# Performance work log

Hardware: AMD Instinct MI355X
Metric: run time of the kernel (lower is better)

Reference implementation:

```python
import jax, jax.numpy as jnp
import numpy as np

N_HEAD = 16

def setup_inputs() -> dict:
    key = jax.random.key(0)
    k1, k2, k3, k4, k5 = jax.random.split(key, 5)
    B, T, C = 8, 2048, 1024
    hs = C // N_HEAD  # 64
    return {
        "ids": jax.random.normal(k1, (B, T, C), dtype=jnp.float32),
        "qkv_w": jax.random.normal(k2, (3 * hs, C), dtype=jnp.float32) * (C ** -0.5),
        "qkv_b": jax.random.normal(k3, (3 * hs,), dtype=jnp.float32) * 0.02,
        "proj_w": jax.random.normal(k4, (C, C), dtype=jnp.float32) * (C ** -0.5),
        "proj_b": jax.random.normal(k5, (C,), dtype=jnp.float32) * 0.02,
    }

def reference(ids, qkv_w, qkv_b, proj_w, proj_b):
    B, T, C = ids.shape
    hs = qkv_w.shape[0] // 3  # head_size
    # All heads share the same qkv Linear (input is replicated per-head in the
    # original), so compute one head and tile at the end.
    qkv = ids @ qkv_w.T + qkv_b                      # [B,T,3*hs]
    q, k, v = jnp.split(qkv, 3, axis=-1)             # each [B,T,hs]
    wei = jnp.einsum('btd,bsd->bts', q, k)           # [B,T,T]
    tril = jnp.tril(jnp.ones((T, T), dtype=bool))
    wei = jnp.where(tril, wei, jnp.float32(0.0))     # causal mask (no softmax)
    out_h = jnp.einsum('bts,bsd->btd', wei, v)       # [B,T,hs]
    out = jnp.tile(out_h, (1, 1, N_HEAD))            # identical heads concatenated
    return out @ proj_w.T + proj_b                   # [B,T,C]
```

## Files before the change

### kernel.cpp

```cpp
#include <hip/hip_runtime.h>
#include <hip/hip_bf16.h>

#define Bsz 8
#define Tsz 2048
#define Csz 1024
#define HSsz 64
#define NQ 192

typedef __attribute__((ext_vector_type(8))) short short8v;
typedef __attribute__((ext_vector_type(4))) float f32x4;
typedef unsigned short ushortT;
typedef unsigned int uintT;

__device__ __forceinline__ unsigned int f2bf(float f) {
    union { float f; unsigned int u; } v; v.f = f;
    return (v.u + 0x7fffu + ((v.u >> 16) & 1u)) >> 16;
}

__device__ __forceinline__ unsigned int pk2bf(float lo, float hi) {
    union { __hip_bfloat162 h2; unsigned int u; } cv;
    cv.h2 = __float22bfloat162_rn(float2{lo, hi});
    return cv.u;
}

__global__ __launch_bounds__(256) void k_prep(const float* __restrict__ qw,
                                              const float* __restrict__ pw,
                                              ushortT* __restrict__ wB,
                                              ushortT* __restrict__ w2a) {
    const int blk = blockIdx.x;
    if (blk < 96) {
        int idx = blk * 256 + threadIdx.x;
        int l = idx & 63;
        int ksjt = idx >> 6;
        int jt = ksjt % 12, ks = ksjt / 12;
        int j = jt * 16 + (l & 15);
        int k = ks * 32 + (l >> 4) * 8;
        const float* src = &qw[j * Csz + k];
        float4 a = *(const float4*)src;
        float4 b = *(const float4*)(src + 4);
        uint4 o;
        o.x = f2bf(a.x) | (f2bf(a.y) << 16);
        o.y = f2bf(a.z) | (f2bf(a.w) << 16);
        o.z = f2bf(b.x) | (f2bf(b.y) << 16);
        o.w = f2bf(b.z) | (f2bf(b.w) << 16);
        *(uint4*)&wB[(size_t)idx * 8] = o;
    } else {
        int idx = (blk - 96) * 256 + threadIdx.x;
        int l = idx & 63;
        int rest = idx >> 6;
        int m = rest & 63, ks = rest >> 6;
        int c = m * 16 + (l & 15);
        int d0 = ks * 32 + (l >> 4) * 8;
        float s0 = 0, s1 = 0, s2 = 0, s3 = 0, s4 = 0, s5 = 0, s6 = 0, s7 = 0;
#pragma unroll
        for (int hh = 0; hh < 16; ++hh) {
            const float* p = &pw[c * Csz + hh * HSsz + d0];
            float4 x = *(const float4*)p;
            float4 y = *(const float4*)(p + 4);
            s0 += x.x; s1 += x.y; s2 += x.z; s3 += x.w;
            s4 += y.x; s5 += y.y; s6 += y.z; s7 += y.w;
        }
        uint4 o;
        o.x = f2bf(s0) | (f2bf(s1) << 16);
        o.y = f2bf(s2) | (f2bf(s3) << 16);
        o.z = f2bf(s4) | (f2bf(s5) << 16);
        o.w = f2bf(s6) | (f2bf(s7) << 16);
        *(uint4*)&w2a[(size_t)idx * 8] = o;
    }
}

__global__ __launch_bounds__(512, 4) void k_qkv_mfma(const float* __restrict__ ids,
                                                     const ushortT* __restrict__ wB,
                                                     const float* __restrict__ bias,
                                                     ushortT* __restrict__ Qf,
                                                     ushortT* __restrict__ Kf,
                                                     ushortT* __restrict__ Vf) {
    __shared__ float sA[2][32 * 68];
    uintT* Lqk = (uintT*)&sA[0][0];
    uintT* Lv  = Lqk + 32 * 68;

    const int tid = threadIdx.x;
    const int wv  = tid >> 6;
    const int l   = tid & 63;
    const int wm  = wv >> 2;
    const int wn  = wv & 3;
    const int lg  = l >> 4, ll = l & 15;

    const int row0 = blockIdx.x * 32;

    const int srow = tid >> 4;
    const int scol = (tid & 15) * 4;
    const float* gsrc = ids + (size_t)(row0 + srow) * Csz + scol;

    const int afrow = wm * 16 + ll;

    f32x4 acc[3];
    acc[0] = acc[1] = acc[2] = (f32x4){0.f, 0.f, 0.f, 0.f};

    float4 st = *(const float4*)gsrc;

    const ushortT* bbase_p = wB + ((size_t)(wn * 3) * 64 + l) * 8;

    for (int c = 0; c < 16; ++c) {
        float* bufp = &sA[c & 1][0];
        *(float4*)&bufp[srow * 68 + scol] = st;
        if (c < 15) st = *(const float4*)(gsrc + (c + 1) * 64);
        __syncthreads();

        const ushortT* bp = bbase_p + (size_t)(2 * c) * 6144;
        short8v b00 = *(const short8v*)(bp);
        short8v b01 = *(const short8v*)(bp + 512);
        short8v b02 = *(const short8v*)(bp + 1024);
        short8v b10 = *(const short8v*)(bp + 6144);
        short8v b11 = *(const short8v*)(bp + 6144 + 512);
        short8v b12 = *(const short8v*)(bp + 6144 + 1024);

        const float* ap = &bufp[afrow * 68 + lg * 8];
        float4 a00 = *(const float4*)(ap);
        float4 a01 = *(const float4*)(ap + 4);
        float4 a10 = *(const float4*)(ap + 32);
        float4 a11 = *(const float4*)(ap + 36);

        union { short8v s; unsigned int u[4]; } af0, af1;
        af0.u[0] = pk2bf(a00.x, a00.y); af0.u[1] = pk2bf(a00.z, a00.w);
        af0.u[2] = pk2bf(a01.x, a01.y); af0.u[3] = pk2bf(a01.z, a01.w);
        af1.u[0] = pk2bf(a10.x, a10.y); af1.u[1] = pk2bf(a10.z, a10.w);
        af1.u[2] = pk2bf(a11.x, a11.y); af1.u[3] = pk2bf(a11.z, a11.w);

        acc[0] = __builtin_amdgcn_mfma_f32_16x16x32_bf16(af0.s, b00, acc[0], 0, 0, 0);
        acc[1] = __builtin_amdgcn_mfma_f32_16x16x32_bf16(af0.s, b01, acc[1], 0, 0, 0);
        acc[2] = __builtin_amdgcn_mfma_f32_16x16x32_bf16(af0.s, b02, acc[2], 0, 0, 0);
        acc[0] = __builtin_amdgcn_mfma_f32_16x16x32_bf16(af1.s, b10, acc[0], 0, 0, 0);
        acc[1] = __builtin_amdgcn_mfma_f32_16x16x32_bf16(af1.s, b11, acc[1], 0, 0, 0);
        acc[2] = __builtin_amdgcn_mfma_f32_16x16x32_bf16(af1.s, b12, acc[2], 0, 0, 0);

        __syncthreads();
    }

    const int crow_l = wm * 16 + lg * 4;
    ushortT* L16 = (ushortT*)Lqk;
#pragma unroll
    for (int n = 0; n < 3; ++n) {
        const int jb = wn * 3 + n;
        const int j  = jb * 16 + ll;
        const float bj = bias[j];
        float v0 = acc[n][0] + bj, v1 = acc[n][1] + bj;
        float v2 = acc[n][2] + bj, v3 = acc[n][3] + bj;
        if (jb < 8) {
            ushortT* p = &L16[crow_l * 136 + j];
            p[0]   = (ushortT)f2bf(v0);
            p[136] = (ushortT)f2bf(v1);
            p[272] = (ushortT)f2bf(v2);
            p[408] = (ushortT)f2bf(v3);
        } else {
            uintT* p = &Lv[(j - 128) * 20 + (crow_l >> 1)];
            p[0] = pk2bf(v0, v1);
            p[1] = pk2bf(v2, v3);
        }
    }
    __syncthreads();

    const int l2 = tid & 63, ll2 = l2 & 15, lg2 = l2 >> 4;
    if (tid < 256) {
        const int ks = (tid >> 6) & 1, m = tid >> 7;
        uint4 q = *(const uint4*)&Lqk[(m * 16 + ll2) * 68 + ks * 16 + lg2 * 4];
        *(uint4*)&Qf[(((size_t)(row0 >> 4) + m) * 2 + ks) * 512 + l2 * 8] = q;
        const int n = tid >> 6;
        uint4 v = *(const uint4*)&Lv[(n * 16 + ll2) * 20 + lg2 * 4];
        const int bb = row0 >> 11, s32 = (row0 >> 5) & 63;
        *(uint4*)&Vf[((((size_t)bb * 64 + s32) * 4 + n) * 64 + l2) * 8] = v;
    } else {
        const int ks = (tid >> 6) & 1, m = (tid >> 7) & 1;
        uint4 k = *(const uint4*)&Lqk[(m * 16 + ll2) * 68 + 32 + ks * 16 + lg2 * 4];
        *(uint4*)&Kf[(((size_t)(row0 >> 4) + m) * 2 + ks) * 512 + l2 * 8] = k;
    }
}

__global__ __launch_bounds__(256, 3) void k_attn_mfma(const ushortT* __restrict__ Qf,
                                                      const ushortT* __restrict__ Kf,
                                                      const ushortT* __restrict__ Vf,
                                                      ushortT* __restrict__ hf) {
    __shared__ uintT su[4 * 2 * 16 * 36];
    __shared__ float s_o[4][32 * 68];

    const int tid = threadIdx.x;
    const int w  = tid >> 6;
    const int l  = tid & 63;
    const int lg = l >> 4;
    const int ll = l & 15;

    const int u = blockIdx.x;
    const int b = u / 48;
    const int r = u - b * 48;

    int si, sub, nsub;
    const bool heavy = (r < 32);
    if (heavy) { si = 63 - r; sub = w; nsub = 4; }
    else {
        const int rr = r - 32;
        si = (w < 2) ? (31 - rr) : rr;
        sub = w & 1; nsub = 2;
    }
    const int nT  = (si >> 1) + 1;
    const int qn  = nT / nsub, rem = nT % nsub;
    const int t0  = sub * qn + (sub < rem ? sub : rem);
    const int cnt = qn + (sub < rem ? 1 : 0);

    const int gq = b * 128 + si * 2;

    short8v qf[2][2];
#pragma unroll
    for (int mt = 0; mt < 2; ++mt)
#pragma unroll
        for (int ks = 0; ks < 2; ++ks)
            qf[mt][ks] = *(const short8v*)&Qf[(((size_t)gq + mt) * 2 + ks) * 512 + l * 8];

    f32x4 oacc[2][4];
#pragma unroll
    for (int mt = 0; mt < 2; ++mt)
#pragma unroll
        for (int n = 0; n < 4; ++n) oacc[mt][n] = (f32x4){0.f, 0.f, 0.f, 0.f};

    for (int tile = t0; tile < t0 + cnt; ++tile) {
        const int gs = b * 128 + tile * 4;
        short8v kf[4][2];
#pragma unroll
        for (int ms = 0; ms < 4; ++ms) {
            const ushortT* kp = &Kf[(((size_t)gs + ms) * 2) * 512 + l * 8];
            kf[ms][0] = *(const short8v*)kp;
            kf[ms][1] = *(const short8v*)(kp + 512);
        }
        f32x4 sacc[4][2];
#pragma unroll
        for (int ms = 0; ms < 4; ++ms)
#pragma unroll
            for (int mt = 0; mt < 2; ++mt) sacc[ms][mt] = (f32x4){0.f, 0.f, 0.f, 0.f};
#pragma unroll
        for (int ms = 0; ms < 4; ++ms)
#pragma unroll
            for (int mt = 0; mt < 2; ++mt) {
                sacc[ms][mt] = __builtin_amdgcn_mfma_f32_16x16x32_bf16(kf[ms][0], qf[mt][0], sacc[ms][mt], 0, 0, 0);
                sacc[ms][mt] = __builtin_amdgcn_mfma_f32_16x16x32_bf16(kf[ms][1], qf[mt][1], sacc[ms][mt], 0, 0, 0);
            }
        if (tile == nT - 1) {
#pragma unroll
            for (int ms = 0; ms < 4; ++ms)
#pragma unroll
                for (int mt = 0; mt < 2; ++mt) {
                    const int tg = si * 32 + mt * 16 + ll;
#pragma unroll
                    for (int rr2 = 0; rr2 < 4; ++rr2) {
                        int sg = tile * 64 + ms * 16 + 4 * lg + rr2;
                        if (sg > tg) sacc[ms][mt][rr2] = 0.f;
                    }
                }
        }
#pragma unroll
        for (int mt = 0; mt < 2; ++mt)
#pragma unroll
            for (int ms = 0; ms < 4; ++ms) {
                uint2 pk;
                pk.x = pk2bf(sacc[ms][mt][0], sacc[ms][mt][1]);
                pk.y = pk2bf(sacc[ms][mt][2], sacc[ms][mt][3]);
                *(uint2*)&su[((w * 2 + mt) * 16 + ll) * 36 + ms * 8 + 2 * lg] = pk;
            }
        union { uint4 u4; short8v s; } pa[2][2];
#pragma unroll
        for (int mt = 0; mt < 2; ++mt)
#pragma unroll
            for (int h = 0; h < 2; ++h)
                pa[mt][h].u4 = *(const uint4*)&su[((w * 2 + mt) * 16 + ll) * 36 + h * 16 + lg * 4];

        const int gv = b * 64 + tile * 2;
        short8v vf[2][4];
#pragma unroll
        for (int h = 0; h < 2; ++h)
#pragma unroll
            for (int n = 0; n < 4; ++n)
                vf[h][n] = *(const short8v*)&Vf[((((size_t)gv + h) * 4 + n) * 64 + l) * 8];
#pragma unroll
        for (int mt = 0; mt < 2; ++mt)
#pragma unroll
            for (int n = 0; n < 4; ++n) {
                oacc[mt][n] = __builtin_amdgcn_mfma_f32_16x16x32_bf16(pa[mt][0].s, vf[0][n], oacc[mt][n], 0, 0, 0);
                oacc[mt][n] = __builtin_amdgcn_mfma_f32_16x16x32_bf16(pa[mt][1].s, vf[1][n], oacc[mt][n], 0, 0, 0);
            }
    }

#pragma unroll
    for (int mt = 0; mt < 2; ++mt)
#pragma unroll
        for (int n = 0; n < 4; ++n)
#pragma unroll
            for (int rr2 = 0; rr2 < 4; ++rr2)
                s_o[w][(mt * 16 + 4 * lg + rr2) * 68 + 16 * n + ll] = oacc[mt][n][rr2];
    __syncthreads();

    const int l2 = tid & 63, ll2 = l2 & 15, lg2 = l2 >> 4;
    const int ks = (tid >> 6) & 1, mt = tid >> 7;
    const int t = mt * 16 + ll2, dd = ks * 32 + lg2 * 8;
    if (heavy) {
        float4 A = {0, 0, 0, 0}, B2 = {0, 0, 0, 0};
#pragma unroll
        for (int w2 = 0; w2 < 4; ++w2) {
            const float4 x = *(const float4*)&s_o[w2][t * 68 + dd];
            const float4 y = *(const float4*)&s_o[w2][t * 68 + dd + 4];
            A.x += x.x; A.y += x.y; A.z += x.z; A.w += x.w;
            B2.x += y.x; B2.y += y.y; B2.z += y.z; B2.w += y.w;
        }
        uint4 o;
        o.x = pk2bf(A.x, A.y);  o.y = pk2bf(A.z, A.w);
        o.z = pk2bf(B2.x, B2.y); o.w = pk2bf(B2.z, B2.w);
        *(uint4*)&hf[(((size_t)(b * 128 + si * 2) + mt) * 2 + ks) * 512 + l2 * 8] = o;
    } else {
        const int rr = r - 32;
        const int sa = 31 - rr, sb = rr;
        float4 A = {0, 0, 0, 0}, B2 = {0, 0, 0, 0};
#pragma unroll
        for (int w2 = 0; w2 < 2; ++w2) {
            const float4 x = *(const float4*)&s_o[w2][t * 68 + dd];
            const float4 y = *(const float4*)&s_o[w2][t * 68 + dd + 4];
            A.x += x.x; A.y += x.y; A.z += x.z; A.w += x.w;
            B2.x += y.x; B2.y += y.y; B2.z += y.z; B2.w += y.w;
        }
        uint4 o;
        o.x = pk2bf(A.x, A.y);  o.y = pk2bf(A.z, A.w);
        o.z = pk2bf(B2.x, B2.y); o.w = pk2bf(B2.z, B2.w);
        *(uint4*)&hf[(((size_t)(b * 128 + sa * 2) + mt) * 2 + ks) * 512 + l2 * 8] = o;
        float4 C = {0, 0, 0, 0}, D2 = {0, 0, 0, 0};
#pragma unroll
        for (int w2 = 2; w2 < 4; ++w2) {
            const float4 x = *(const float4*)&s_o[w2][t * 68 + dd];
            const float4 y = *(const float4*)&s_o[w2][t * 68 + dd + 4];
            C.x += x.x; C.y += x.y; C.z += x.z; C.w += x.w;
            D2.x += y.x; D2.y += y.y; D2.z += y.z; D2.w += y.w;
        }
        uint4 o2;
        o2.x = pk2bf(C.x, C.y);  o2.y = pk2bf(C.z, C.w);
        o2.z = pk2bf(D2.x, D2.y); o2.w = pk2bf(D2.z, D2.w);
        *(uint4*)&hf[(((size_t)(b * 128 + sb * 2) + mt) * 2 + ks) * 512 + l2 * 8] = o2;
    }
}

__global__ __launch_bounds__(256) void k_proj_mfma(const ushortT* __restrict__ hf,
                                                   const ushortT* __restrict__ w2a,
                                                   const float* __restrict__ pb,
                                                   float* __restrict__ out) {
    const int tid = threadIdx.x;
    const int w = tid >> 6, l = tid & 63;
    const int t0 = blockIdx.x * 16;
    const size_t M = blockIdx.x;

    short8v hb0 = *(const short8v*)&hf[(M * 2 + 0) * 512 + l * 8];
    short8v hb1 = *(const short8v*)&hf[(M * 2 + 1) * 512 + l * 8];

    const int row = (l >> 4) * 4;
    const int tcol = l & 15;
    const size_t outrow = (size_t)(t0 + tcol) * Csz;

#pragma unroll 2
    for (int m = w * 16; m < w * 16 + 16; ++m) {
        const ushortT* ap = w2a + (size_t)(m * 64 + l) * 8;
        short8v a0 = *(const short8v*)ap;
        short8v a1 = *(const short8v*)(ap + 32768);
        f32x4 acc = (f32x4){0.f, 0.f, 0.f, 0.f};
        acc = __builtin_amdgcn_mfma_f32_16x16x32_bf16(a0, hb0, acc, 0, 0, 0);
        acc = __builtin_amdgcn_mfma_f32_16x16x32_bf16(a1, hb1, acc, 0, 0, 0);
        const int c0 = m * 16 + row;
        const float4 pv = *(const float4*)&pb[c0];
        float4 o;
        o.x = acc[0] + pv.x; o.y = acc[1] + pv.y;
        o.z = acc[2] + pv.z; o.w = acc[3] + pv.w;
        *(float4*)&out[outrow + c0] = o;
    }
}

extern "C" void kernel_launch(void* const* d_in, const int* in_sizes, int n_in,
                              void* d_out, int out_size, void* d_ws, size_t ws_size,
                              hipStream_t stream) {
    const float* ids    = (const float*)d_in[0];
    const float* qkv_w  = (const float*)d_in[1];
    const float* qkv_b  = (const float*)d_in[2];
    const float* proj_w = (const float*)d_in[3];
    const float* proj_b = (const float*)d_in[4];
    float* out = (float*)d_out;

    ushortT* Qf  = (ushortT*)d_ws;
    ushortT* Kf  = Qf + 16384 * HSsz;
    ushortT* Vf  = Kf + 16384 * HSsz;
    ushortT* hf  = Vf + 16384 * HSsz;
    ushortT* wB  = hf + 16384 * HSsz;
    ushortT* w2a = wB + 196608;

    hipLaunchKernelGGL(k_prep,      dim3(128),  dim3(256), 0, stream, qkv_w, proj_w, wB, w2a);
    hipLaunchKernelGGL(k_qkv_mfma,  dim3(512),  dim3(512), 0, stream, ids, wB, qkv_b, Qf, Kf, Vf);
    hipLaunchKernelGGL(k_attn_mfma, dim3(384),  dim3(256), 0, stream, Qf, Kf, Vf, hf);
    hipLaunchKernelGGL(k_proj_mfma, dim3(1024), dim3(256), 0, stream, hf, w2a, proj_b, out);
}
```

Before: 62.81 us.

## Fuse output projection into attention kernel and widen QKV K-chunks

The output projection now runs inside the attention kernel. Each block reduces its per-wave partial outputs into bf16 MFMA fragments held in registers and multiplies them directly by the projection weights. This removes the intermediate hf buffer round trip through global memory and one kernel launch. Separately, the QKV GEMM now stages 128-column chunks with a single barrier per iteration, halving loop trips and barriers. The cost is that the large fp32 output store is now spread over only 384 attention blocks instead of 1024 dedicated blocks, which may reduce parallelism for the store-bound projection.

```diff
diff --git a/kernel.cpp b/kernel.cpp
--- a/kernel.cpp
+++ b/kernel.cpp
@@ -75,7 +75,7 @@
                                                      ushortT* __restrict__ Qf,
                                                      ushortT* __restrict__ Kf,
                                                      ushortT* __restrict__ Vf) {
-    __shared__ float sA[2][32 * 68];
+    __shared__ float sA[2][32 * 132];
     uintT* Lqk = (uintT*)&sA[0][0];
     uintT* Lv  = Lqk + 32 * 68;
 
@@ -89,7 +89,7 @@
     const int row0 = blockIdx.x * 32;
 
     const int srow = tid >> 4;
-    const int scol = (tid & 15) * 4;
+    const int scol = (tid & 15) * 8;
     const float* gsrc = ids + (size_t)(row0 + srow) * Csz + scol;
 
     const int afrow = wm * 16 + ll;
@@ -97,45 +97,41 @@
     f32x4 acc[3];
     acc[0] = acc[1] = acc[2] = (f32x4){0.f, 0.f, 0.f, 0.f};
 
-    float4 st = *(const float4*)gsrc;
+    float4 st0 = *(const float4*)gsrc;
+    float4 st1 = *(const float4*)(gsrc + 4);
 
     const ushortT* bbase_p = wB + ((size_t)(wn * 3) * 64 + l) * 8;
 
-    for (int c = 0; c < 16; ++c) {
+    for (int c = 0; c < 8; ++c) {
         float* bufp = &sA[c & 1][0];
-        *(float4*)&bufp[srow * 68 + scol] = st;
-        if (c < 15) st = *(const float4*)(gsrc + (c + 1) * 64);
+        float* wp = &bufp[srow * 132 + scol];
+        *(float4*)wp = st0;
+        *(float4*)(wp + 4) = st1;
         __syncthreads();
-
-        const ushortT* bp = bbase_p + (size_t)(2 * c) * 6144;
-        short8v b00 = *(const short8v*)(bp);
-        short8v b01 = *(const short8v*)(bp + 512);
-        short8v b02 = *(const short8v*)(bp + 1024);
-        short8v b10 = *(const short8v*)(bp + 6144);
-        short8v b11 = *(const short8v*)(bp + 6144 + 512);
-        short8v b12 = *(const short8v*)(bp + 6144 + 1024);
-
-        const float* ap = &bufp[afrow * 68 + lg * 8];
-        float4 a00 = *(const float4*)(ap);
-        float4 a01 = *(const float4*)(ap + 4);
-        float4 a10 = *(const float4*)(ap + 32);
-        float4 a11 = *(const float4*)(ap + 36);
-
-        union { short8v s; unsigned int u[4]; } af0, af1;
-        af0.u[0] = pk2bf(a00.x, a00.y); af0.u[1] = pk2bf(a00.z, a00.w);
-        af0.u[2] = pk2bf(a01.x, a01.y); af0.u[3] = pk2bf(a01.z, a01.w);
-        af1.u[0] = pk2bf(a10.x, a10.y); af1.u[1] = pk2bf(a10.z, a10.w);
-        af1.u[2] = pk2bf(a11.x, a11.y); af1.u[3] = pk2bf(a11.z, a11.w);
-
-        acc[0] = __builtin_amdgcn_mfma_f32_16x16x32_bf16(af0.s, b00, acc[0], 0, 0, 0);
-        acc[1] = __builtin_amdgcn_mfma_f32_16x16x32_bf16(af0.s, b01, acc[1], 0, 0, 0);
-        acc[2] = __builtin_amdgcn_mfma_f32_16x16x32_bf16(af0.s, b02, acc[2], 0, 0, 0);
-        acc[0] = __builtin_amdgcn_mfma_f32_16x16x32_bf16(af1.s, b10, acc[0], 0, 0, 0);
-        acc[1] = __builtin_amdgcn_mfma_f32_16x16x32_bf16(af1.s, b11, acc[1], 0, 0, 0);
-        acc[2] = __builtin_amdgcn_mfma_f32_16x16x32_bf16(af1.s, b12, acc[2], 0, 0, 0);
-
-        __syncthreads();
-    }
+        if (c < 7) {
+            st0 = *(const float4*)(gsrc + (c + 1) * 128);
+            st1 = *(const float4*)(gsrc + (c + 1) * 128 + 4);
+        }
+#pragma unroll
+        for (int kk = 0; kk < 4; ++kk) {
+            const ushortT* bp = bbase_p + (size_t)(4 * c + kk) * 6144;
+            short8v b0 = *(const short8v*)(bp);
+            short8v b1 = *(const short8v*)(bp + 512);
+            short8v b2 = *(const short8v*)(bp + 1024);
+
+            const float* ap = &bufp[afrow * 132 + kk * 32 + lg * 8];
+            float4 a0 = *(const float4*)ap;
+            float4 a1 = *(const float4*)(ap + 4);
+            union { short8v s; unsigned int u[4]; } af;
+            af.u[0] = pk2bf(a0.x, a0.y); af.u[1] = pk2bf(a0.z, a0.w);
+            af.u[2] = pk2bf(a1.x, a1.y); af.u[3] = pk2bf(a1.z, a1.w);
+
+            acc[0] = __builtin_amdgcn_mfma_f32_16x16x32_bf16(af.s, b0, acc[0], 0, 0, 0);
+            acc[1] = __builtin_amdgcn_mfma_f32_16x16x32_bf16(af.s, b1, acc[1], 0, 0, 0);
+            acc[2] = __builtin_amdgcn_mfma_f32_16x16x32_bf16(af.s, b2, acc[2], 0, 0, 0);
+        }
+    }
+    __syncthreads();
 
     const int crow_l = wm * 16 + lg * 4;
     ushortT* L16 = (ushortT*)Lqk;
@@ -176,10 +172,12 @@
     }
 }
 
-__global__ __launch_bounds__(256, 3) void k_attn_mfma(const ushortT* __restrict__ Qf,
+__global__ __launch_bounds__(256, 3) void k_attn_proj(const ushortT* __restrict__ Qf,
                                                       const ushortT* __restrict__ Kf,
                                                       const ushortT* __restrict__ Vf,
-                                                      ushortT* __restrict__ hf) {
+                                                      const ushortT* __restrict__ w2a,
+                                                      const float* __restrict__ pb,
+                                                      float* __restrict__ out) {
     __shared__ uintT su[4 * 2 * 16 * 36];
     __shared__ float s_o[4][32 * 68];
 
@@ -296,82 +294,52 @@
                 s_o[w][(mt * 16 + 4 * lg + rr2) * 68 + 16 * n + ll] = oacc[mt][n][rr2];
     __syncthreads();
 
-    const int l2 = tid & 63, ll2 = l2 & 15, lg2 = l2 >> 4;
-    const int ks = (tid >> 6) & 1, mt = tid >> 7;
-    const int t = mt * 16 + ll2, dd = ks * 32 + lg2 * 8;
-    if (heavy) {
-        float4 A = {0, 0, 0, 0}, B2 = {0, 0, 0, 0};
-#pragma unroll
-        for (int w2 = 0; w2 < 4; ++w2) {
-            const float4 x = *(const float4*)&s_o[w2][t * 68 + dd];
-            const float4 y = *(const float4*)&s_o[w2][t * 68 + dd + 4];
-            A.x += x.x; A.y += x.y; A.z += x.z; A.w += x.w;
-            B2.x += y.x; B2.y += y.y; B2.z += y.z; B2.w += y.w;
-        }
-        uint4 o;
-        o.x = pk2bf(A.x, A.y);  o.y = pk2bf(A.z, A.w);
-        o.z = pk2bf(B2.x, B2.y); o.w = pk2bf(B2.z, B2.w);
-        *(uint4*)&hf[(((size_t)(b * 128 + si * 2) + mt) * 2 + ks) * 512 + l2 * 8] = o;
-    } else {
+    int pstrip, nsum, wb0, mstart, mcount;
+    if (heavy) { pstrip = si; nsum = 4; wb0 = 0; mstart = w * 16; mcount = 16; }
+    else {
         const int rr = r - 32;
-        const int sa = 31 - rr, sb = rr;
-        float4 A = {0, 0, 0, 0}, B2 = {0, 0, 0, 0};
-#pragma unroll
-        for (int w2 = 0; w2 < 2; ++w2) {
-            const float4 x = *(const float4*)&s_o[w2][t * 68 + dd];
-            const float4 y = *(const float4*)&s_o[w2][t * 68 + dd + 4];
-            A.x += x.x; A.y += x.y; A.z += x.z; A.w += x.w;
-            B2.x += y.x; B2.y += y.y; B2.z += y.z; B2.w += y.w;
-        }
-        uint4 o;
-        o.x = pk2bf(A.x, A.y);  o.y = pk2bf(A.z, A.w);
-        o.z = pk2bf(B2.x, B2.y); o.w = pk2bf(B2.z, B2.w);
-        *(uint4*)&hf[(((size_t)(b * 128 + sa * 2) + mt) * 2 + ks) * 512 + l2 * 8] = o;
-        float4 C = {0, 0, 0, 0}, D2 = {0, 0, 0, 0};
-#pragma unroll
-        for (int w2 = 2; w2 < 4; ++w2) {
-            const float4 x = *(const float4*)&s_o[w2][t * 68 + dd];
-            const float4 y = *(const float4*)&s_o[w2][t * 68 + dd + 4];
-            C.x += x.x; C.y += x.y; C.z += x.z; C.w += x.w;
-            D2.x += y.x; D2.y += y.y; D2.z += y.z; D2.w += y.w;
-        }
-        uint4 o2;
-        o2.x = pk2bf(C.x, C.y);  o2.y = pk2bf(C.z, C.w);
-        o2.z = pk2bf(D2.x, D2.y); o2.w = pk2bf(D2.z, D2.w);
-        *(uint4*)&hf[(((size_t)(b * 128 + sb * 2) + mt) * 2 + ks) * 512 + l2 * 8] = o2;
-    }
-}
-
-__global__ __launch_bounds__(256) void k_proj_mfma(const ushortT* __restrict__ hf,
-                                                   const ushortT* __restrict__ w2a,
-                                                   const float* __restrict__ pb,
-                                                   float* __restrict__ out) {
-    const int tid = threadIdx.x;
-    const int w = tid >> 6, l = tid & 63;
-    const int t0 = blockIdx.x * 16;
-    const size_t M = blockIdx.x;
-
-    short8v hb0 = *(const short8v*)&hf[(M * 2 + 0) * 512 + l * 8];
-    short8v hb1 = *(const short8v*)&hf[(M * 2 + 1) * 512 + l * 8];
-
-    const int row = (l >> 4) * 4;
-    const int tcol = l & 15;
-    const size_t outrow = (size_t)(t0 + tcol) * Csz;
-
-#pragma unroll 2
-    for (int m = w * 16; m < w * 16 + 16; ++m) {
+        pstrip = (w < 2) ? (31 - rr) : rr;
+        nsum = 2; wb0 = (w < 2) ? 0 : 2;
+        mstart = (w & 1) * 32; mcount = 32;
+    }
+
+    union { short8v s; unsigned int u[4]; } hbf[2][2];
+#pragma unroll
+    for (int mt = 0; mt < 2; ++mt)
+#pragma unroll
+        for (int ks = 0; ks < 2; ++ks) {
+            float4 A = {0.f, 0.f, 0.f, 0.f}, B2 = {0.f, 0.f, 0.f, 0.f};
+            for (int w2 = wb0; w2 < wb0 + nsum; ++w2) {
+                const float* p = &s_o[w2][(mt * 16 + ll) * 68 + ks * 32 + lg * 8];
+                const float4 x = *(const float4*)p;
+                const float4 y = *(const float4*)(p + 4);
+                A.x += x.x; A.y += x.y; A.z += x.z; A.w += x.w;
+                B2.x += y.x; B2.y += y.y; B2.z += y.z; B2.w += y.w;
+            }
+            hbf[mt][ks].u[0] = pk2bf(A.x, A.y);
+            hbf[mt][ks].u[1] = pk2bf(A.z, A.w);
+            hbf[mt][ks].u[2] = pk2bf(B2.x, B2.y);
+            hbf[mt][ks].u[3] = pk2bf(B2.z, B2.w);
+        }
+
+    const int gt = b * Tsz + pstrip * 32;
+    const int crow = lg * 4;
+#pragma unroll 4
+    for (int m = mstart; m < mstart + mcount; ++m) {
         const ushortT* ap = w2a + (size_t)(m * 64 + l) * 8;
         short8v a0 = *(const short8v*)ap;
         short8v a1 = *(const short8v*)(ap + 32768);
-        f32x4 acc = (f32x4){0.f, 0.f, 0.f, 0.f};
-        acc = __builtin_amdgcn_mfma_f32_16x16x32_bf16(a0, hb0, acc, 0, 0, 0);
-        acc = __builtin_amdgcn_mfma_f32_16x16x32_bf16(a1, hb1, acc, 0, 0, 0);
-        const int c0 = m * 16 + row;
-        const float4 pv = *(const float4*)&pb[c0];
-        float4 o;
-        o.x = acc[0] + pv.x; o.y = acc[1] + pv.y;
-        o.z = acc[2] + pv.z; o.w = acc[3] + pv.w;
-        *(float4*)&out[outrow + c0] = o;
+        const float4 pv = *(const float4*)&pb[m * 16 + crow];
+#pragma unroll
+        for (int mt = 0; mt < 2; ++mt) {
+            f32x4 acc = (f32x4){0.f, 0.f, 0.f, 0.f};
+            acc = __builtin_amdgcn_mfma_f32_16x16x32_bf16(a0, hbf[mt][0].s, acc, 0, 0, 0);
+            acc = __builtin_amdgcn_mfma_f32_16x16x32_bf16(a1, hbf[mt][1].s, acc, 0, 0, 0);
+            float4 o;
+            o.x = acc[0] + pv.x; o.y = acc[1] + pv.y;
+            o.z = acc[2] + pv.z; o.w = acc[3] + pv.w;
+            *(float4*)&out[(size_t)(gt + mt * 16 + ll) * Csz + m * 16 + crow] = o;
+        }
     }
 }
 
@@ -388,12 +356,10 @@
     ushortT* Qf  = (ushortT*)d_ws;
     ushortT* Kf  = Qf + 16384 * HSsz;
     ushortT* Vf  = Kf + 16384 * HSsz;
-    ushortT* hf  = Vf + 16384 * HSsz;
-    ushortT* wB  = hf + 16384 * HSsz;
+    ushortT* wB  = Vf + 16384 * HSsz;
     ushortT* w2a = wB + 196608;
 
-    hipLaunchKernelGGL(k_prep,      dim3(128),  dim3(256), 0, stream, qkv_w, proj_w, wB, w2a);
-    hipLaunchKernelGGL(k_qkv_mfma,  dim3(512),  dim3(512), 0, stream, ids, wB, qkv_b, Qf, Kf, Vf);
-    hipLaunchKernelGGL(k_attn_mfma, dim3(384),  dim3(256), 0, stream, Qf, Kf, Vf, hf);
-    hipLaunchKernelGGL(k_proj_mfma, dim3(1024), dim3(256), 0, stream, hf, w2a, proj_b, out);
-}
+    hipLaunchKernelGGL(k_prep,      dim3(128), dim3(256), 0, stream, qkv_w, proj_w, wB, w2a);
+    hipLaunchKernelGGL(k_qkv_mfma,  dim3(512), dim3(512), 0, stream, ids, wB, qkv_b, Qf, Kf, Vf);
+    hipLaunchKernelGGL(k_attn_proj, dim3(384), dim3(256), 0, stream, Qf, Kf, Vf, w2a, proj_b, out);
+}
```

Result: slower. 72.83 us (+15.9%).
